# Kernel tuning notes

Measured on AMD Instinct MI355X. Metric: run time of the kernel, lower is better.

Reference implementation:

```python
import jax, jax.numpy as jnp
import numpy as np

V, E, H, ENC = 10000, 512, 512, 2048
B, T, P = 64, 64, 196


def setup_inputs() -> dict:
    key = jax.random.key(0)
    ks = jax.random.split(key, 12)
    s = 0.02
    return {
        "encoder_out": jax.random.normal(ks[0], (B, P, ENC), jnp.float32),
        "targets": jax.random.randint(ks[1], (B, T), 0, V),
        "embedding": jax.random.normal(ks[2], (V, E), jnp.float32) * s,
        "W_ih": jax.random.normal(ks[3], (4 * H, E), jnp.float32) * s,
        "W_hh": jax.random.normal(ks[4], (4 * H, H), jnp.float32) * s,
        "b_ih": jnp.zeros((4 * H,), jnp.float32),
        "b_hh": jnp.zeros((4 * H,), jnp.float32),
        "Wh": jax.random.normal(ks[5], (H, ENC), jnp.float32) * s,
        "bh": jnp.zeros((H,), jnp.float32),
        "Wc": jax.random.normal(ks[6], (H, ENC), jnp.float32) * s,
        "bc": jnp.zeros((H,), jnp.float32),
        "Wout": jax.random.normal(ks[7], (V, H), jnp.float32) * s,
        "bout": jnp.zeros((V,), jnp.float32),
    }


def reference(encoder_out, targets, embedding, W_ih, W_hh, b_ih, b_hh, Wh, bh, Wc, bc, Wout, bout):
    # init hidden state from mean-pooled encoder features
    mean_enc = encoder_out.mean(axis=1)                      # [B, ENC]
    h0 = jnp.tanh(mean_enc @ Wh.T + bh)                      # [B, H]
    c0 = jnp.tanh(mean_enc @ Wc.T + bc)                      # [B, H]

    Bsz, Tlen = targets.shape
    # teacher forcing (ratio=1.0): input at step t is targets[:, t-1]
    emb = embedding[targets[:, :-1]]                         # [B, T-1, E]
    # precompute input-dependent gate pre-activations (dropout = eval identity)
    xg = jnp.einsum('bte,ge->btg', emb, W_ih) + b_ih + b_hh  # [B, T-1, 4H]

    def step(carry, x):
        h, c = carry
        gates = x + h @ W_hh.T                               # [B, 4H]
        i, f, g, o = jnp.split(gates, 4, axis=-1)
        i = jax.nn.sigmoid(i)
        f = jax.nn.sigmoid(f)
        g = jnp.tanh(g)
        o = jax.nn.sigmoid(o)
        c = f * c + i * g
        h = o * jnp.tanh(c)
        out = h @ Wout.T + bout                              # [B, V]
        return (h, c), out

    _, outs = jax.lax.scan(step, (h0, c0), jnp.swapaxes(xg, 0, 1))
    outs = jnp.swapaxes(outs, 0, 1)                          # [B, T-1, V]
    zeros0 = jnp.zeros((Bsz, 1, outs.shape[-1]), outs.dtype)  # step 0 untouched
    return jnp.concatenate([zeros0, outs], axis=1)           # [B, T, V]
```

## Files before the change

kernel.cpp:

```cpp
#include <hip/hip_runtime.h>

typedef __bf16 bf16x8 __attribute__((ext_vector_type(8)));
typedef float f32x4 __attribute__((ext_vector_type(4)));

static __device__ __forceinline__ unsigned short f2bf(float f) {
    unsigned u = __builtin_bit_cast(unsigned, f);
    unsigned r = u + 0x7fffu + ((u >> 16) & 1u);
    return (unsigned short)(r >> 16);
}

#define GLD_LDS16(g, l) __builtin_amdgcn_global_load_lds( \
    (const __attribute__((address_space(1))) unsigned int*)(const void*)(g), \
    (__attribute__((address_space(3))) unsigned int*)(void*)(l), 16, 0, 0)

__global__ __launch_bounds__(256) void k_prep(
    const float* Wih, const float* Whh, const float* Wh, const float* Wc,
    const float* Wout, const float* emb, const int* targets, const float* enc,
    unsigned short* Wih_b, unsigned short* Whh_b, unsigned short* Wh_b,
    unsigned short* Wc_b, unsigned short* Wout_b, unsigned short* Aemb,
    float* out, int* ctrs, float* ps, unsigned short* mean_b)
{
    const int bid = blockIdx.x, tid = threadIdx.x;

    if (bid < 2048) {
        long f = ((long)bid * 256 + tid) * 8;
        int a = (int)(f >> 20);
        long off = f & 1048575;
        const float* s = (a == 0) ? Wih : (a == 1) ? Whh : (a == 2) ? Wh : Wc;
        unsigned short* d = (a == 0) ? Wih_b : (a == 1) ? Whh_b : (a == 2) ? Wh_b : Wc_b;
        float4 v0 = *(const float4*)(s + off);
        float4 v1 = *(const float4*)(s + off + 4);
        unsigned short r[8] = {f2bf(v0.x), f2bf(v0.y), f2bf(v0.z), f2bf(v0.w),
                               f2bf(v1.x), f2bf(v1.y), f2bf(v1.z), f2bf(v1.w)};
        *(uint4*)(d + off) = *(uint4*)r;
        return;
    }
    if (bid < 4548) {
        long f = ((long)(bid - 2048) * 256 + tid) * 8;
        float4 v0 = *(const float4*)(Wout + f);
        float4 v1 = *(const float4*)(Wout + f + 4);
        unsigned short r[8] = {f2bf(v0.x), f2bf(v0.y), f2bf(v0.z), f2bf(v0.w),
                               f2bf(v1.x), f2bf(v1.y), f2bf(v1.z), f2bf(v1.w)};
        *(uint4*)(Wout_b + f) = *(uint4*)r;
        return;
    }
    if (bid < 5556) {
        unsigned t = (unsigned)(bid - 4548) * 256 + tid;
        unsigned row = t >> 6;
        unsigned col = (t & 63) * 8;
        unsigned b = row / 63u, tt = row - b * 63u;
        int trg = targets[b * 64 + tt];
        const float* s = emb + (long)trg * 512 + col;
        float4 v0 = *(const float4*)(s);
        float4 v1 = *(const float4*)(s + 4);
        unsigned short r[8] = {f2bf(v0.x), f2bf(v0.y), f2bf(v0.z), f2bf(v0.w),
                               f2bf(v1.x), f2bf(v1.y), f2bf(v1.z), f2bf(v1.w)};
        *(uint4*)(Aemb + (long)row * 512 + col) = *(uint4*)r;
        return;
    }
    if (bid < 6181) {
        unsigned idx = ((unsigned)(bid - 5556) * 256 + tid) * 4;
        unsigned b = idx / 10000u, v = idx - b * 10000u;
        *(float4*)(out + (long)b * 640000 + v) = (float4){0.f, 0.f, 0.f, 0.f};
        return;
    }
    if (bid < 6246) {
        int rel = bid - 6181;
        if (rel < 64) {
            unsigned idx = ((unsigned)rel * 256 + tid) * 4;
            *(float4*)(ps + idx) = (float4){0.f, 0.f, 0.f, 0.f};
        } else {
            ctrs[tid] = 0;
        }
        return;
    }
    {
        unsigned idx = (unsigned)(bid - 6246) * 256 + tid;
        unsigned b = idx >> 11, c = idx & 2047;
        const float* base = enc + (long)b * 196 * 2048 + c;
        float s0 = 0.f, s1 = 0.f, s2 = 0.f, s3 = 0.f;
        for (int p = 0; p < 196; p += 4) {
            s0 += base[(long)(p + 0) * 2048];
            s1 += base[(long)(p + 1) * 2048];
            s2 += base[(long)(p + 2) * 2048];
            s3 += base[(long)(p + 3) * 2048];
        }
        mean_b[(long)b * 2048 + c] = f2bf((s0 + s1 + s2 + s3) * (1.f / 196.f));
    }
}

__global__ __launch_bounds__(256) void k_gemm2(
    const unsigned short* mean_b, const unsigned short* Whb, const unsigned short* Wcb,
    float* ps,
    const unsigned short* Aemb, const unsigned short* Wihb,
    const float* bih, const float* bhh, float* xg)
{
    __shared__ __align__(16) char smem[16384];
    const int bid = blockIdx.x, tid = threadIdx.x;
    const int w = tid >> 6, lane = tid & 63, quad = lane >> 4, l16 = lane & 15;

    if (bid < 64) {
        unsigned short* As = (unsigned short*)smem;
        unsigned short* Bs = (unsigned short*)(smem + 5120);
        const int n0 = (bid & 15) * 64;
        const int kc = (bid >> 4) * 16;
        const int r = tid >> 2, seg = tid & 3;
        f32x4 acc[4];
#pragma unroll
        for (int i = 0; i < 4; i++) acc[i] = (f32x4){0.f, 0.f, 0.f, 0.f};

        for (int kb = kc; kb < kc + 16; kb++) {
            int k0 = kb * 32;
            *(uint4*)&As[r * 40 + seg * 8] = *(const uint4*)&mean_b[(long)r * 2048 + k0 + seg * 8];
            int ngr = n0 + r;
            const unsigned short* bsrc = (ngr < 512) ? (Whb + (long)ngr * 2048)
                                                     : (Wcb + (long)(ngr - 512) * 2048);
            *(uint4*)&Bs[r * 40 + seg * 8] = *(const uint4*)&bsrc[k0 + seg * 8];
            __syncthreads();
            bf16x8 bfr = *(const bf16x8*)&Bs[(16 * w + l16) * 40 + quad * 8];
#pragma unroll
            for (int mt = 0; mt < 4; mt++) {
                bf16x8 af = *(const bf16x8*)&As[(mt * 16 + l16) * 40 + quad * 8];
                acc[mt] = __builtin_amdgcn_mfma_f32_16x16x32_bf16(af, bfr, acc[mt], 0, 0, 0);
            }
            __syncthreads();
        }
        int ng = n0 + 16 * w + l16;
#pragma unroll
        for (int mt = 0; mt < 4; mt++) {
#pragma unroll
            for (int rr = 0; rr < 4; rr++) {
                int m = mt * 16 + quad * 4 + rr;
                atomicAdd(&ps[(long)m * 1024 + ng], acc[mt][rr]);
            }
        }
        return;
    }

    unsigned short* As = (unsigned short*)smem;
    unsigned short* Bs = (unsigned short*)(smem + 8192);
    const int rel = bid - 64;
    const int n0 = (rel & 15) * 128, m0 = (rel >> 4) * 128;
    const int wm = w >> 1, wn = w & 1;
    const int gr = lane >> 2, gc = (lane & 3) * 8;

    f32x4 acc[4][4];
#pragma unroll
    for (int i = 0; i < 4; i++)
#pragma unroll
        for (int j = 0; j < 4; j++) acc[i][j] = (f32x4){0.f, 0.f, 0.f, 0.f};

    for (int kb = 0; kb < 16; kb++) {
        int k0 = kb * 32;
#pragma unroll
        for (int p = 0; p < 2; p++) {
            int rowa = m0 + p * 64 + w * 16 + gr;
            GLD_LDS16(Aemb + (long)rowa * 512 + k0 + gc, As + (p * 64 + w * 16) * 32);
            int rowb = n0 + p * 64 + w * 16 + gr;
            GLD_LDS16(Wihb + (long)rowb * 512 + k0 + gc, Bs + (p * 64 + w * 16) * 32);
        }
        __syncthreads();
        bf16x8 af[4], bf[4];
#pragma unroll
        for (int mt = 0; mt < 4; mt++)
            af[mt] = *(const bf16x8*)&As[(wm * 64 + mt * 16 + l16) * 32 + quad * 8];
#pragma unroll
        for (int nt = 0; nt < 4; nt++)
            bf[nt] = *(const bf16x8*)&Bs[(wn * 64 + nt * 16 + l16) * 32 + quad * 8];
#pragma unroll
        for (int mt = 0; mt < 4; mt++)
#pragma unroll
            for (int nt = 0; nt < 4; nt++)
                acc[mt][nt] = __builtin_amdgcn_mfma_f32_16x16x32_bf16(af[mt], bf[nt], acc[mt][nt], 0, 0, 0);
        __syncthreads();
    }
#pragma unroll
    for (int nt = 0; nt < 4; nt++) {
        int n = n0 + wn * 64 + nt * 16 + l16;
        float bias = bih[n] + bhh[n];
#pragma unroll
        for (int mt = 0; mt < 4; mt++) {
#pragma unroll
            for (int rr = 0; rr < 4; rr++) {
                int r = m0 + wm * 64 + mt * 16 + quad * 4 + rr;
                if (r < 4032) xg[(long)r * 2048 + n] = acc[mt][nt][rr] + bias;
            }
        }
    }
}

__global__ __launch_bounds__(256) void k_fin(
    const float* ps, const float* bh, const float* bc,
    unsigned short* Hbuf, float* c0buf)
{
    int i = blockIdx.x * 256 + threadIdx.x;
    int m = i >> 10, ng = i & 1023;
    int j = ng & 511;
    float bias = (ng < 512) ? bh[j] : bc[j];
    float v = tanhf(ps[i] + bias);
    if (ng < 512) Hbuf[(long)m * 512 + j] = f2bf(v);
    else          c0buf[(long)m * 512 + j] = v;
}

__global__ __launch_bounds__(256, 1) void k_scan(
    const unsigned short* Whh_b, const float* xg, const float* c0buf,
    unsigned short* Hbuf, int* ctrs)
{
    __shared__ unsigned short Wlds[128 * 520];
    __shared__ unsigned short hs[16 * 520];
    __shared__ float gs[16 * 133];
    const int tid = threadIdx.x;
    const int gid = blockIdx.x;
    const int b0 = (gid & 3) * 16;
    const int j0 = (gid >> 2) * 32;
    const int w = tid >> 6, lane = tid & 63, quad = lane >> 4, l16 = lane & 15;
    const int m = tid >> 4, u0 = (tid & 15) * 2;

    for (int nrel = w; nrel < 128; nrel += 4) {
        int q = nrel >> 5, u = nrel & 31;
        *(uint4*)&Wlds[nrel * 520 + lane * 8] =
            *(const uint4*)&Whh_b[(long)(q * 512 + j0 + u) * 512 + lane * 8];
    }
    float2 cr = *(const float2*)&c0buf[(long)(b0 + m) * 512 + j0 + u0];
    float c0v = cr.x, c1v = cr.y;
    int* ctr = ctrs + (gid & 3) * 64;
    __syncthreads();

    for (int s = 1; s < 64; s++) {
        const float* xb = xg + ((long)(b0 + m) * 63 + (s - 1)) * 2048 + j0 + u0;
        float2 xv0 = *(const float2*)(xb + 0);
        float2 xv1 = *(const float2*)(xb + 512);
        float2 xv2 = *(const float2*)(xb + 1024);
        float2 xv3 = *(const float2*)(xb + 1536);

        const unsigned* hsrc = (const unsigned*)(Hbuf + ((long)(s - 1) * 64 + b0) * 512);
        unsigned hv[16];
#pragma unroll
        for (int j = 0; j < 16; j++)
            hv[j] = __hip_atomic_load(hsrc + j * 256 + tid, __ATOMIC_RELAXED,
                                      __HIP_MEMORY_SCOPE_AGENT);
#pragma unroll
        for (int j = 0; j < 16; j++)
            *(unsigned*)&hs[j * 520 + tid * 2] = hv[j];
        __syncthreads();

        f32x4 acc0 = (f32x4){0.f, 0.f, 0.f, 0.f};
        f32x4 acc1 = (f32x4){0.f, 0.f, 0.f, 0.f};
#pragma unroll
        for (int kk = 0; kk < 16; kk++) {
            bf16x8 a  = *(const bf16x8*)&hs[l16 * 520 + kk * 32 + quad * 8];
            bf16x8 bA = *(const bf16x8*)&Wlds[(32 * w + l16) * 520 + kk * 32 + quad * 8];
            bf16x8 bB = *(const bf16x8*)&Wlds[(32 * w + 16 + l16) * 520 + kk * 32 + quad * 8];
            acc0 = __builtin_amdgcn_mfma_f32_16x16x32_bf16(a, bA, acc0, 0, 0, 0);
            acc1 = __builtin_amdgcn_mfma_f32_16x16x32_bf16(a, bB, acc1, 0, 0, 0);
        }
#pragma unroll
        for (int rr = 0; rr < 4; rr++) {
            gs[(quad * 4 + rr) * 133 + 32 * w + l16] = acc0[rr];
            gs[(quad * 4 + rr) * 133 + 32 * w + 16 + l16] = acc1[rr];
        }
        __syncthreads();

        float gi0 = gs[m * 133 + u0]          + xv0.x;
        float gi1 = gs[m * 133 + u0 + 1]      + xv0.y;
        float gf0 = gs[m * 133 + 32 + u0]     + xv1.x;
        float gf1 = gs[m * 133 + 33 + u0]     + xv1.y;
        float gg0 = gs[m * 133 + 64 + u0]     + xv2.x;
        float gg1 = gs[m * 133 + 65 + u0]     + xv2.y;
        float go0 = gs[m * 133 + 96 + u0]     + xv3.x;
        float go1 = gs[m * 133 + 97 + u0]     + xv3.y;
        float cn0 = (1.f / (1.f + __expf(-gf0))) * c0v + (1.f / (1.f + __expf(-gi0))) * tanhf(gg0);
        float cn1 = (1.f / (1.f + __expf(-gf1))) * c1v + (1.f / (1.f + __expf(-gi1))) * tanhf(gg1);
        c0v = cn0; c1v = cn1;
        float h0v = (1.f / (1.f + __expf(-go0))) * tanhf(cn0);
        float h1v = (1.f / (1.f + __expf(-go1))) * tanhf(cn1);
        unsigned hp = (unsigned)f2bf(h0v) | ((unsigned)f2bf(h1v) << 16);
        __hip_atomic_store((unsigned*)(Hbuf + ((long)s * 64 + b0 + m) * 512 + j0 + u0), hp,
                           __ATOMIC_RELAXED, __HIP_MEMORY_SCOPE_AGENT);

        if (s < 63) {
            __syncthreads();
            if (tid == 0) {
                __hip_atomic_fetch_add(ctr, 1, __ATOMIC_RELEASE, __HIP_MEMORY_SCOPE_AGENT);
                int target = s * 16;
                while (__hip_atomic_load(ctr, __ATOMIC_RELAXED, __HIP_MEMORY_SCOPE_AGENT) < target) {}
            }
            __syncthreads();
        }
    }
}

__global__ __launch_bounds__(256) void k_out(
    const unsigned short* A, const unsigned short* Wob, const float* bout, float* out)
{
    __shared__ unsigned short As[128 * 32];
    __shared__ unsigned short Bs[128 * 32];
    const int tid = threadIdx.x;
    const int tile = (blockIdx.x & 7) * 316 + (blockIdx.x >> 3);
    const int n0 = (tile >> 5) * 128, m0 = (tile & 31) * 128;
    const int w = tid >> 6, lane = tid & 63, quad = lane >> 4, l16 = lane & 15;
    const int wm = w >> 1, wn = w & 1;
    const int gr = lane >> 2, gc = (lane & 3) * 8;

    f32x4 acc[4][4];
#pragma unroll
    for (int i = 0; i < 4; i++)
#pragma unroll
        for (int j = 0; j < 4; j++) acc[i][j] = (f32x4){0.f, 0.f, 0.f, 0.f};

    for (int kb = 0; kb < 16; kb++) {
        int k0 = kb * 32;
#pragma unroll
        for (int p = 0; p < 2; p++) {
            int rowa = m0 + p * 64 + w * 16 + gr;
            GLD_LDS16(A + (long)rowa * 512 + k0 + gc, As + (p * 64 + w * 16) * 32);
            int rowb = n0 + p * 64 + w * 16 + gr;
            GLD_LDS16(Wob + (long)rowb * 512 + k0 + gc, Bs + (p * 64 + w * 16) * 32);
        }
        __syncthreads();
        bf16x8 af[4], bf[4];
#pragma unroll
        for (int mt = 0; mt < 4; mt++)
            af[mt] = *(const bf16x8*)&As[(wm * 64 + mt * 16 + l16) * 32 + quad * 8];
#pragma unroll
        for (int nt = 0; nt < 4; nt++)
            bf[nt] = *(const bf16x8*)&Bs[(wn * 64 + nt * 16 + l16) * 32 + quad * 8];
#pragma unroll
        for (int mt = 0; mt < 4; mt++)
#pragma unroll
            for (int nt = 0; nt < 4; nt++)
                acc[mt][nt] = __builtin_amdgcn_mfma_f32_16x16x32_bf16(af[mt], bf[nt], acc[mt][nt], 0, 0, 0);
        __syncthreads();
    }
#pragma unroll
    for (int nt = 0; nt < 4; nt++) {
        int n = n0 + wn * 64 + nt * 16 + l16;
        if (n >= 10000) continue;
        float bias = bout[n];
#pragma unroll
        for (int mt = 0; mt < 4; mt++) {
#pragma unroll
            for (int rr = 0; rr < 4; rr++) {
                int r = m0 + wm * 64 + mt * 16 + quad * 4 + rr;
                if (r < 4032) {
                    int s = (r >> 6) + 1, b = r & 63;
                    out[((long)b * 64 + s) * 10000 + n] = acc[mt][nt][rr] + bias;
                }
            }
        }
    }
}

extern "C" void kernel_launch(void* const* d_in, const int* in_sizes, int n_in,
                              void* d_out, int out_size, void* d_ws, size_t ws_size,
                              hipStream_t stream)
{
    const float* enc     = (const float*)d_in[0];
    const int*   targets = (const int*)d_in[1];
    const float* emb     = (const float*)d_in[2];
    const float* Wih     = (const float*)d_in[3];
    const float* Whh     = (const float*)d_in[4];
    const float* bih     = (const float*)d_in[5];
    const float* bhh     = (const float*)d_in[6];
    const float* Wh      = (const float*)d_in[7];
    const float* bh      = (const float*)d_in[8];
    const float* Wc      = (const float*)d_in[9];
    const float* bc      = (const float*)d_in[10];
    const float* Wout    = (const float*)d_in[11];
    const float* bout    = (const float*)d_in[12];
    float* out = (float*)d_out;

    char* ws = (char*)d_ws;
    size_t off = 0;
    auto alloc = [&](size_t bytes) {
        void* p = ws + off;
        off = (off + bytes + 255) & ~(size_t)255;
        return p;
    };
    unsigned short* mean_b = (unsigned short*)alloc((size_t)64 * 2048 * 2);
    unsigned short* Wih_b  = (unsigned short*)alloc((size_t)2048 * 512 * 2);
    unsigned short* Whh_b  = (unsigned short*)alloc((size_t)2048 * 512 * 2);
    unsigned short* Wh_b   = (unsigned short*)alloc((size_t)512 * 2048 * 2);
    unsigned short* Wc_b   = (unsigned short*)alloc((size_t)512 * 2048 * 2);
    unsigned short* Wout_b = (unsigned short*)alloc((size_t)10000 * 512 * 2);
    unsigned short* Aemb   = (unsigned short*)alloc((size_t)(4032 + 64) * 512 * 2);
    float*          xg     = (float*)alloc((size_t)4032 * 2048 * 4);
    unsigned short* Hbuf   = (unsigned short*)alloc((size_t)(64 * 64 + 64) * 512 * 2);
    float*          c0buf  = (float*)alloc((size_t)64 * 512 * 4);
    int*            ctrs   = (int*)alloc(256 * 4);
    float*          ps     = (float*)alloc((size_t)64 * 1024 * 4);

    k_prep<<<6758, 256, 0, stream>>>(Wih, Whh, Wh, Wc, Wout, emb, targets, enc,
                                     Wih_b, Whh_b, Wh_b, Wc_b, Wout_b, Aemb,
                                     out, ctrs, ps, mean_b);
    k_gemm2<<<576, 256, 0, stream>>>(mean_b, Wh_b, Wc_b, ps,
                                     Aemb, Wih_b, bih, bhh, xg);
    k_fin<<<256, 256, 0, stream>>>(ps, bh, bc, Hbuf, c0buf);
    k_scan<<<64, 256, 0, stream>>>(Whh_b, xg, c0buf, Hbuf, ctrs);
    k_out<<<2528, 256, 0, stream>>>(Hbuf + 64 * 512, Wout_b, bout, out);
}
```

Before: 627.4 us.

## Fold h0/c0 init into scan kernel and widen output GEMM M-tile

Removes the k_fin launch. The scan kernel now computes tanh(ps+bias) itself, writing h0 straight into shared memory and c0 into registers, so the first step skips its global h load. Separately, the output-projection GEMM tile grows to 256x128. Each block reuses its loaded Wout tile across two A halves, which halves the grid and the B-matrix traffic, at the cost of more accumulator registers and possibly lower occupancy.

```diff
diff --git a/kernel.cpp b/kernel.cpp
--- a/kernel.cpp
+++ b/kernel.cpp
@@ -189,21 +189,9 @@
     }
 }
 
-__global__ __launch_bounds__(256) void k_fin(
+__global__ __launch_bounds__(256, 1) void k_scan(
+    const unsigned short* Whh_b, const float* xg,
     const float* ps, const float* bh, const float* bc,
-    unsigned short* Hbuf, float* c0buf)
-{
-    int i = blockIdx.x * 256 + threadIdx.x;
-    int m = i >> 10, ng = i & 1023;
-    int j = ng & 511;
-    float bias = (ng < 512) ? bh[j] : bc[j];
-    float v = tanhf(ps[i] + bias);
-    if (ng < 512) Hbuf[(long)m * 512 + j] = f2bf(v);
-    else          c0buf[(long)m * 512 + j] = v;
-}
-
-__global__ __launch_bounds__(256, 1) void k_scan(
-    const unsigned short* Whh_b, const float* xg, const float* c0buf,
     unsigned short* Hbuf, int* ctrs)
 {
     __shared__ unsigned short Wlds[128 * 520];
@@ -221,8 +209,31 @@
         *(uint4*)&Wlds[nrel * 520 + lane * 8] =
             *(const uint4*)&Whh_b[(long)(q * 512 + j0 + u) * 512 + lane * 8];
     }
-    float2 cr = *(const float2*)&c0buf[(long)(b0 + m) * 512 + j0 + u0];
-    float c0v = cr.x, c1v = cr.y;
+    {
+        int j = tid >> 4;
+        int ub = (tid & 15) * 32;
+        const float* prow = ps + (long)(b0 + j) * 1024;
+#pragma unroll
+        for (int q = 0; q < 4; q++) {
+            float4 a  = *(const float4*)(prow + ub + q * 8);
+            float4 b  = *(const float4*)(prow + ub + q * 8 + 4);
+            float4 ba = *(const float4*)(bh + ub + q * 8);
+            float4 bb = *(const float4*)(bh + ub + q * 8 + 4);
+            unsigned short r[8] = {
+                f2bf(tanhf(a.x + ba.x)), f2bf(tanhf(a.y + ba.y)),
+                f2bf(tanhf(a.z + ba.z)), f2bf(tanhf(a.w + ba.w)),
+                f2bf(tanhf(b.x + bb.x)), f2bf(tanhf(b.y + bb.y)),
+                f2bf(tanhf(b.z + bb.z)), f2bf(tanhf(b.w + bb.w))};
+            *(uint4*)&hs[j * 520 + ub + q * 8] = *(uint4*)r;
+        }
+    }
+    float c0v, c1v;
+    {
+        float2 pc  = *(const float2*)&ps[(long)(b0 + m) * 1024 + 512 + j0 + u0];
+        float2 bcv = *(const float2*)&bc[j0 + u0];
+        c0v = tanhf(pc.x + bcv.x);
+        c1v = tanhf(pc.y + bcv.y);
+    }
     int* ctr = ctrs + (gid & 3) * 64;
     __syncthreads();
 
@@ -233,15 +244,17 @@
         float2 xv2 = *(const float2*)(xb + 1024);
         float2 xv3 = *(const float2*)(xb + 1536);
 
-        const unsigned* hsrc = (const unsigned*)(Hbuf + ((long)(s - 1) * 64 + b0) * 512);
-        unsigned hv[16];
-#pragma unroll
-        for (int j = 0; j < 16; j++)
-            hv[j] = __hip_atomic_load(hsrc + j * 256 + tid, __ATOMIC_RELAXED,
-                                      __HIP_MEMORY_SCOPE_AGENT);
-#pragma unroll
-        for (int j = 0; j < 16; j++)
-            *(unsigned*)&hs[j * 520 + tid * 2] = hv[j];
+        if (s > 1) {
+            const unsigned* hsrc = (const unsigned*)(Hbuf + ((long)(s - 1) * 64 + b0) * 512);
+            unsigned hv[16];
+#pragma unroll
+            for (int j = 0; j < 16; j++)
+                hv[j] = __hip_atomic_load(hsrc + j * 256 + tid, __ATOMIC_RELAXED,
+                                          __HIP_MEMORY_SCOPE_AGENT);
+#pragma unroll
+            for (int j = 0; j < 16; j++)
+                *(unsigned*)&hs[j * 520 + tid * 2] = hv[j];
+        }
         __syncthreads();
 
         f32x4 acc0 = (f32x4){0.f, 0.f, 0.f, 0.f};
@@ -293,58 +306,69 @@
 __global__ __launch_bounds__(256) void k_out(
     const unsigned short* A, const unsigned short* Wob, const float* bout, float* out)
 {
-    __shared__ unsigned short As[128 * 32];
+    __shared__ unsigned short As[2][128 * 32];
     __shared__ unsigned short Bs[128 * 32];
     const int tid = threadIdx.x;
-    const int tile = (blockIdx.x & 7) * 316 + (blockIdx.x >> 3);
-    const int n0 = (tile >> 5) * 128, m0 = (tile & 31) * 128;
+    const int tile = (blockIdx.x & 7) * 158 + (blockIdx.x >> 3);
+    const int n0 = (tile >> 4) * 128;
+    const int m0 = (tile & 15) * 256;
     const int w = tid >> 6, lane = tid & 63, quad = lane >> 4, l16 = lane & 15;
     const int wm = w >> 1, wn = w & 1;
     const int gr = lane >> 2, gc = (lane & 3) * 8;
 
-    f32x4 acc[4][4];
-#pragma unroll
-    for (int i = 0; i < 4; i++)
-#pragma unroll
-        for (int j = 0; j < 4; j++) acc[i][j] = (f32x4){0.f, 0.f, 0.f, 0.f};
+    f32x4 acc[2][4][4];
+#pragma unroll
+    for (int h = 0; h < 2; h++)
+#pragma unroll
+        for (int i = 0; i < 4; i++)
+#pragma unroll
+            for (int j = 0; j < 4; j++) acc[h][i][j] = (f32x4){0.f, 0.f, 0.f, 0.f};
 
     for (int kb = 0; kb < 16; kb++) {
         int k0 = kb * 32;
 #pragma unroll
         for (int p = 0; p < 2; p++) {
-            int rowa = m0 + p * 64 + w * 16 + gr;
-            GLD_LDS16(A + (long)rowa * 512 + k0 + gc, As + (p * 64 + w * 16) * 32);
             int rowb = n0 + p * 64 + w * 16 + gr;
             GLD_LDS16(Wob + (long)rowb * 512 + k0 + gc, Bs + (p * 64 + w * 16) * 32);
-        }
-        __syncthreads();
-        bf16x8 af[4], bf[4];
-#pragma unroll
-        for (int mt = 0; mt < 4; mt++)
-            af[mt] = *(const bf16x8*)&As[(wm * 64 + mt * 16 + l16) * 32 + quad * 8];
+#pragma unroll
+            for (int h = 0; h < 2; h++) {
+                int rowa = m0 + h * 128 + p * 64 + w * 16 + gr;
+                GLD_LDS16(A + (long)rowa * 512 + k0 + gc, As[h] + (p * 64 + w * 16) * 32);
+            }
+        }
+        __syncthreads();
+        bf16x8 bf[4];
 #pragma unroll
         for (int nt = 0; nt < 4; nt++)
             bf[nt] = *(const bf16x8*)&Bs[(wn * 64 + nt * 16 + l16) * 32 + quad * 8];
 #pragma unroll
-        for (int mt = 0; mt < 4; mt++)
-#pragma unroll
-            for (int nt = 0; nt < 4; nt++)
-                acc[mt][nt] = __builtin_amdgcn_mfma_f32_16x16x32_bf16(af[mt], bf[nt], acc[mt][nt], 0, 0, 0);
-        __syncthreads();
-    }
-#pragma unroll
-    for (int nt = 0; nt < 4; nt++) {
-        int n = n0 + wn * 64 + nt * 16 + l16;
-        if (n >= 10000) continue;
-        float bias = bout[n];
-#pragma unroll
-        for (int mt = 0; mt < 4; mt++) {
-#pragma unroll
-            for (int rr = 0; rr < 4; rr++) {
-                int r = m0 + wm * 64 + mt * 16 + quad * 4 + rr;
-                if (r < 4032) {
-                    int s = (r >> 6) + 1, b = r & 63;
-                    out[((long)b * 64 + s) * 10000 + n] = acc[mt][nt][rr] + bias;
+        for (int h = 0; h < 2; h++) {
+#pragma unroll
+            for (int mt = 0; mt < 4; mt++) {
+                bf16x8 af = *(const bf16x8*)&As[h][(wm * 64 + mt * 16 + l16) * 32 + quad * 8];
+#pragma unroll
+                for (int nt = 0; nt < 4; nt++)
+                    acc[h][mt][nt] = __builtin_amdgcn_mfma_f32_16x16x32_bf16(af, bf[nt], acc[h][mt][nt], 0, 0, 0);
+            }
+        }
+        __syncthreads();
+    }
+#pragma unroll
+    for (int h = 0; h < 2; h++) {
+#pragma unroll
+        for (int nt = 0; nt < 4; nt++) {
+            int n = n0 + wn * 64 + nt * 16 + l16;
+            if (n >= 10000) continue;
+            float bias = bout[n];
+#pragma unroll
+            for (int mt = 0; mt < 4; mt++) {
+#pragma unroll
+                for (int rr = 0; rr < 4; rr++) {
+                    int r = m0 + h * 128 + wm * 64 + mt * 16 + quad * 4 + rr;
+                    if (r < 4032) {
+                        int s = (r >> 6) + 1, b = r & 63;
+                        out[((long)b * 64 + s) * 10000 + n] = acc[h][mt][nt][rr] + bias;
+                    }
                 }
             }
         }
@@ -386,7 +410,6 @@
     unsigned short* Aemb   = (unsigned short*)alloc((size_t)(4032 + 64) * 512 * 2);
     float*          xg     = (float*)alloc((size_t)4032 * 2048 * 4);
     unsigned short* Hbuf   = (unsigned short*)alloc((size_t)(64 * 64 + 64) * 512 * 2);
-    float*          c0buf  = (float*)alloc((size_t)64 * 512 * 4);
     int*            ctrs   = (int*)alloc(256 * 4);
     float*          ps     = (float*)alloc((size_t)64 * 1024 * 4);
 
@@ -395,7 +418,6 @@
                                      out, ctrs, ps, mean_b);
     k_gemm2<<<576, 256, 0, stream>>>(mean_b, Wh_b, Wc_b, ps,
                                      Aemb, Wih_b, bih, bhh, xg);
-    k_fin<<<256, 256, 0, stream>>>(ps, bh, bc, Hbuf, c0buf);
-    k_scan<<<64, 256, 0, stream>>>(Whh_b, xg, c0buf, Hbuf, ctrs);
-    k_out<<<2528, 256, 0, stream>>>(Hbuf + 64 * 512, Wout_b, bout, out);
-}
+    k_scan<<<64, 256, 0, stream>>>(Whh_b, xg, ps, bh, bc, Hbuf, ctrs);
+    k_out<<<1264, 256, 0, stream>>>(Hbuf + 64 * 512, Wout_b, bout, out);
+}
```

New measurement: 689.4 us. 9.9% more time.

## Fold h0/c0 init into scan and overlap Wout conversion with recurrence

Applied to the files above, without the earlier changes.

Removes the k_fin kernel: each scan block computes its own h0 tile into LDS and its c0 values directly from the partial sums with tanh, skipping the Hbuf load on the first step. The Wout bf16 conversion and the zeroing of output step 0 move out of k_prep into extra blocks of the scan launch, so they can run on CUs left idle by the 64-block recurrence. This saves one launch and shortens the pre-scan critical path. The risk is that the extra blocks could compete with the scan blocks for memory bandwidth, or delay their scheduling.

```diff
diff --git a/kernel.cpp b/kernel.cpp
--- a/kernel.cpp
+++ b/kernel.cpp
@@ -15,10 +15,10 @@
 
 __global__ __launch_bounds__(256) void k_prep(
     const float* Wih, const float* Whh, const float* Wh, const float* Wc,
-    const float* Wout, const float* emb, const int* targets, const float* enc,
+    const float* emb, const int* targets, const float* enc,
     unsigned short* Wih_b, unsigned short* Whh_b, unsigned short* Wh_b,
-    unsigned short* Wc_b, unsigned short* Wout_b, unsigned short* Aemb,
-    float* out, int* ctrs, float* ps, unsigned short* mean_b)
+    unsigned short* Wc_b, unsigned short* Aemb,
+    int* ctrs, float* ps, unsigned short* mean_b)
 {
     const int bid = blockIdx.x, tid = threadIdx.x;
 
@@ -35,17 +35,8 @@
         *(uint4*)(d + off) = *(uint4*)r;
         return;
     }
-    if (bid < 4548) {
-        long f = ((long)(bid - 2048) * 256 + tid) * 8;
-        float4 v0 = *(const float4*)(Wout + f);
-        float4 v1 = *(const float4*)(Wout + f + 4);
-        unsigned short r[8] = {f2bf(v0.x), f2bf(v0.y), f2bf(v0.z), f2bf(v0.w),
-                               f2bf(v1.x), f2bf(v1.y), f2bf(v1.z), f2bf(v1.w)};
-        *(uint4*)(Wout_b + f) = *(uint4*)r;
-        return;
-    }
-    if (bid < 5556) {
-        unsigned t = (unsigned)(bid - 4548) * 256 + tid;
+    if (bid < 3056) {
+        unsigned t = (unsigned)(bid - 2048) * 256 + tid;
         unsigned row = t >> 6;
         unsigned col = (t & 63) * 8;
         unsigned b = row / 63u, tt = row - b * 63u;
@@ -58,14 +49,8 @@
         *(uint4*)(Aemb + (long)row * 512 + col) = *(uint4*)r;
         return;
     }
-    if (bid < 6181) {
-        unsigned idx = ((unsigned)(bid - 5556) * 256 + tid) * 4;
-        unsigned b = idx / 10000u, v = idx - b * 10000u;
-        *(float4*)(out + (long)b * 640000 + v) = (float4){0.f, 0.f, 0.f, 0.f};
-        return;
-    }
-    if (bid < 6246) {
-        int rel = bid - 6181;
+    if (bid < 3121) {
+        int rel = bid - 3056;
         if (rel < 64) {
             unsigned idx = ((unsigned)rel * 256 + tid) * 4;
             *(float4*)(ps + idx) = (float4){0.f, 0.f, 0.f, 0.f};
@@ -75,7 +60,7 @@
         return;
     }
     {
-        unsigned idx = (unsigned)(bid - 6246) * 256 + tid;
+        unsigned idx = (unsigned)(bid - 3121) * 256 + tid;
         unsigned b = idx >> 11, c = idx & 2047;
         const float* base = enc + (long)b * 196 * 2048 + c;
         float s0 = 0.f, s1 = 0.f, s2 = 0.f, s3 = 0.f;
@@ -189,28 +174,35 @@
     }
 }
 
-__global__ __launch_bounds__(256) void k_fin(
+__global__ __launch_bounds__(256, 1) void k_scan(
+    const unsigned short* Whh_b, const float* xg,
     const float* ps, const float* bh, const float* bc,
-    unsigned short* Hbuf, float* c0buf)
-{
-    int i = blockIdx.x * 256 + threadIdx.x;
-    int m = i >> 10, ng = i & 1023;
-    int j = ng & 511;
-    float bias = (ng < 512) ? bh[j] : bc[j];
-    float v = tanhf(ps[i] + bias);
-    if (ng < 512) Hbuf[(long)m * 512 + j] = f2bf(v);
-    else          c0buf[(long)m * 512 + j] = v;
-}
-
-__global__ __launch_bounds__(256, 1) void k_scan(
-    const unsigned short* Whh_b, const float* xg, const float* c0buf,
-    unsigned short* Hbuf, int* ctrs)
+    unsigned short* Hbuf, int* ctrs,
+    const float* Wout, unsigned short* Wout_b, float* out)
 {
     __shared__ unsigned short Wlds[128 * 520];
     __shared__ unsigned short hs[16 * 520];
     __shared__ float gs[16 * 133];
     const int tid = threadIdx.x;
     const int gid = blockIdx.x;
+
+    if (gid >= 64) {
+        int sb = gid - 64;
+        if (sb < 2500) {
+            long f = ((long)sb * 256 + tid) * 8;
+            float4 v0 = *(const float4*)(Wout + f);
+            float4 v1 = *(const float4*)(Wout + f + 4);
+            unsigned short r[8] = {f2bf(v0.x), f2bf(v0.y), f2bf(v0.z), f2bf(v0.w),
+                                   f2bf(v1.x), f2bf(v1.y), f2bf(v1.z), f2bf(v1.w)};
+            *(uint4*)(Wout_b + f) = *(uint4*)r;
+        } else {
+            unsigned idx = ((unsigned)(sb - 2500) * 256 + tid) * 4;
+            unsigned b = idx / 10000u, v = idx - b * 10000u;
+            *(float4*)(out + (long)b * 640000 + v) = (float4){0.f, 0.f, 0.f, 0.f};
+        }
+        return;
+    }
+
     const int b0 = (gid & 3) * 16;
     const int j0 = (gid >> 2) * 32;
     const int w = tid >> 6, lane = tid & 63, quad = lane >> 4, l16 = lane & 15;
@@ -221,8 +213,31 @@
         *(uint4*)&Wlds[nrel * 520 + lane * 8] =
             *(const uint4*)&Whh_b[(long)(q * 512 + j0 + u) * 512 + lane * 8];
     }
-    float2 cr = *(const float2*)&c0buf[(long)(b0 + m) * 512 + j0 + u0];
-    float c0v = cr.x, c1v = cr.y;
+    {
+        int j = tid >> 4;
+        int ub = (tid & 15) * 32;
+        const float* prow = ps + (long)(b0 + j) * 1024;
+#pragma unroll
+        for (int q = 0; q < 4; q++) {
+            float4 a  = *(const float4*)(prow + ub + q * 8);
+            float4 b  = *(const float4*)(prow + ub + q * 8 + 4);
+            float4 ba = *(const float4*)(bh + ub + q * 8);
+            float4 bb = *(const float4*)(bh + ub + q * 8 + 4);
+            unsigned short r[8] = {
+                f2bf(tanhf(a.x + ba.x)), f2bf(tanhf(a.y + ba.y)),
+                f2bf(tanhf(a.z + ba.z)), f2bf(tanhf(a.w + ba.w)),
+                f2bf(tanhf(b.x + bb.x)), f2bf(tanhf(b.y + bb.y)),
+                f2bf(tanhf(b.z + bb.z)), f2bf(tanhf(b.w + bb.w))};
+            *(uint4*)&hs[j * 520 + ub + q * 8] = *(uint4*)r;
+        }
+    }
+    float c0v, c1v;
+    {
+        float2 pc  = *(const float2*)&ps[(long)(b0 + m) * 1024 + 512 + j0 + u0];
+        float2 bcv = *(const float2*)&bc[j0 + u0];
+        c0v = tanhf(pc.x + bcv.x);
+        c1v = tanhf(pc.y + bcv.y);
+    }
     int* ctr = ctrs + (gid & 3) * 64;
     __syncthreads();
 
@@ -233,15 +248,17 @@
         float2 xv2 = *(const float2*)(xb + 1024);
         float2 xv3 = *(const float2*)(xb + 1536);
 
-        const unsigned* hsrc = (const unsigned*)(Hbuf + ((long)(s - 1) * 64 + b0) * 512);
-        unsigned hv[16];
-#pragma unroll
-        for (int j = 0; j < 16; j++)
-            hv[j] = __hip_atomic_load(hsrc + j * 256 + tid, __ATOMIC_RELAXED,
-                                      __HIP_MEMORY_SCOPE_AGENT);
-#pragma unroll
-        for (int j = 0; j < 16; j++)
-            *(unsigned*)&hs[j * 520 + tid * 2] = hv[j];
+        if (s > 1) {
+            const unsigned* hsrc = (const unsigned*)(Hbuf + ((long)(s - 1) * 64 + b0) * 512);
+            unsigned hv[16];
+#pragma unroll
+            for (int j = 0; j < 16; j++)
+                hv[j] = __hip_atomic_load(hsrc + j * 256 + tid, __ATOMIC_RELAXED,
+                                          __HIP_MEMORY_SCOPE_AGENT);
+#pragma unroll
+            for (int j = 0; j < 16; j++)
+                *(unsigned*)&hs[j * 520 + tid * 2] = hv[j];
+        }
         __syncthreads();
 
         f32x4 acc0 = (f32x4){0.f, 0.f, 0.f, 0.f};
@@ -386,16 +403,15 @@
     unsigned short* Aemb   = (unsigned short*)alloc((size_t)(4032 + 64) * 512 * 2);
     float*          xg     = (float*)alloc((size_t)4032 * 2048 * 4);
     unsigned short* Hbuf   = (unsigned short*)alloc((size_t)(64 * 64 + 64) * 512 * 2);
-    float*          c0buf  = (float*)alloc((size_t)64 * 512 * 4);
     int*            ctrs   = (int*)alloc(256 * 4);
     float*          ps     = (float*)alloc((size_t)64 * 1024 * 4);
 
-    k_prep<<<6758, 256, 0, stream>>>(Wih, Whh, Wh, Wc, Wout, emb, targets, enc,
-                                     Wih_b, Whh_b, Wh_b, Wc_b, Wout_b, Aemb,
-                                     out, ctrs, ps, mean_b);
+    k_prep<<<3633, 256, 0, stream>>>(Wih, Whh, Wh, Wc, emb, targets, enc,
+                                     Wih_b, Whh_b, Wh_b, Wc_b, Aemb,
+                                     ctrs, ps, mean_b);
     k_gemm2<<<576, 256, 0, stream>>>(mean_b, Wh_b, Wc_b, ps,
                                      Aemb, Wih_b, bih, bhh, xg);
-    k_fin<<<256, 256, 0, stream>>>(ps, bh, bc, Hbuf, c0buf);
-    k_scan<<<64, 256, 0, stream>>>(Whh_b, xg, c0buf, Hbuf, ctrs);
+    k_scan<<<64 + 3125, 256, 0, stream>>>(Whh_b, xg, ps, bh, bc, Hbuf, ctrs,
+                                          Wout, Wout_b, out);
     k_out<<<2528, 256, 0, stream>>>(Hbuf + 64 * 512, Wout_b, bout, out);
 }
```

Result: no change. 617.8 us (-1.5%).
